# Performance work log

Measured on AMD Instinct MI355X. Metric: run time of the kernel, lower is better.

## Reference

```python
import jax, jax.numpy as jnp
import numpy as np

N, H, S, R, T = 32768, 512, 8, 64, 12

def setup_inputs() -> dict:
    key = jax.random.key(0)
    ks = jax.random.split(key, 7)
    scale = 1.0 / np.sqrt(H)
    return {
        "encodings": jax.random.normal(ks[0], (N, H), dtype=jnp.float32),
        "domain_encs": jax.random.normal(ks[1], (S, H), dtype=jnp.float32),
        "Us": jax.random.normal(ks[2], (S, H, R), dtype=jnp.float32) * scale,
        "W1": jax.random.normal(ks[3], (S, H, H), dtype=jnp.float32) * scale,
        "b1": jax.random.normal(ks[4], (S, H), dtype=jnp.float32) * 0.01,
        "W2": jax.random.normal(ks[5], (S, H, T), dtype=jnp.float32) * scale,
        "b2": jax.random.normal(ks[6], (S, T), dtype=jnp.float32) * 0.01,
    }

def reference(encodings, domain_encs, Us, W1, b1, W2, b2):
    # Mahalanobis soft routing. Original computes (p-mu) @ (U U^T) @ (p-mu)^T
    # and takes sqrt(diag) -- algebraically identical to project-then-square-sum.
    diff = encodings[None, :, :] - domain_encs[:, None, :]        # [S, N, H]
    proj = jnp.einsum('snh,shr->snr', diff, Us)                   # [S, N, R]
    dist = jnp.sqrt(jnp.sum(proj * proj, axis=-1))                # [S, N]
    alphas = jax.nn.softmax(-dist, axis=0)                        # softmax over sources

    # Per-source classifier: Dropout(eval=identity) -> ReLU -> Linear(H,H)
    # -> Dropout -> ReLU -> Linear(H,T) -> Sigmoid
    h0 = jax.nn.relu(encodings)                                   # [N, H]
    h1 = jax.nn.relu(jnp.einsum('nh,shk->snk', h0, W1) + b1[:, None, :])  # [S, N, H]
    out = jax.nn.sigmoid(jnp.einsum('snk,skt->snt', h1, W2) + b2[:, None, :])  # [S, N, T]

    # Softmax-weighted combine of expert outputs
    return jnp.sum(alphas[:, :, None] * out, axis=0)              # [N, T]
```

## Files before the change

kernel.cpp:

```cpp
#include <hip/hip_runtime.h>
#include <hip/hip_bf16.h>

typedef unsigned short u16;
typedef __bf16 bf16x8 __attribute__((ext_vector_type(8)));
typedef float f32x4 __attribute__((ext_vector_type(4)));

#define NROWS 32768
#define H 512
#define NS 8
#define NR 64
#define NT 12

#define WS_W1T   0
#define WS_UCT   4194304
#define WS_W2T   4718592
#define WS_CVEC  4849664
#define WS_ALPH  4851712

union BFU { __bf16 h; u16 u; };
__device__ __forceinline__ u16 f2bf(float v) { BFU b; b.h = (__bf16)v; return b.u; }

__device__ __forceinline__ void gload16(const u16* g, u16* l) {
  __builtin_amdgcn_global_load_lds(
      (const __attribute__((address_space(1))) unsigned int*)g,
      (__attribute__((address_space(3))) unsigned int*)l, 16, 0, 0);
}

__global__ __launch_bounds__(256) void prep(
    const float* __restrict__ W1, u16* __restrict__ W1T,
    const float* __restrict__ Us, u16* __restrict__ UcatT,
    const float* __restrict__ W2, u16* __restrict__ W2T,
    const float* __restrict__ mu, float* __restrict__ cvec) {
  __shared__ float tile[32][33];
  const int bid = blockIdx.x;
  const int tx = threadIdx.x, ty = threadIdx.y;
  if (bid < 2432) {
    const float* in; u16* out; int Rr, Cc, Cpad, b, r0, c0;
    if (bid < 2048) {
      in = W1; out = W1T; Rr = 512; Cc = 512; Cpad = 512;
      r0 = (bid & 15) * 32; c0 = ((bid >> 4) & 15) * 32; b = bid >> 8;
    } else if (bid < 2304) {
      int t2 = bid - 2048; in = Us; out = UcatT; Rr = 512; Cc = 64; Cpad = 64;
      r0 = (t2 & 15) * 32; c0 = ((t2 >> 4) & 1) * 32; b = t2 >> 5;
    } else {
      int t2 = bid - 2304; in = W2; out = W2T; Rr = 512; Cc = 12; Cpad = 16;
      r0 = (t2 & 15) * 32; c0 = 0; b = t2 >> 4;
    }
#pragma unroll
    for (int i = 0; i < 4; i++) {
      int r = r0 + ty + i * 8, c = c0 + tx;
      float v = 0.f;
      if (r < Rr && c < Cc) v = in[((size_t)b * Rr + r) * Cc + c];
      tile[ty + i * 8][tx] = v;
    }
    __syncthreads();
#pragma unroll
    for (int i = 0; i < 4; i++) {
      int c = c0 + ty + i * 8, r = r0 + tx;
      if (c < Cpad && r < Rr) out[((size_t)b * Cpad + c) * Rr + r] = f2bf(tile[tx][ty + i * 8]);
    }
  } else {
    const int tid = ty * 32 + tx;
    const int idx = (bid - 2432) * 4 + (tid >> 6);
    const int s = idx >> 6, r = idx & 63, t = tid & 63;
    float acc = 0.f;
#pragma unroll
    for (int k = t; k < H; k += 64) acc += mu[s * H + k] * Us[((size_t)s * H + k) * NR + r];
#pragma unroll
    for (int m = 32; m; m >>= 1) acc += __shfl_xor(acc, m, 64);
    if (t == 0) cvec[idx] = acc;
  }
}

__device__ __forceinline__ void stage32r(const u16* __restrict__ g, u16* l, int wave, int lane) {
#pragma unroll
  for (int i = 0; i < 8; i++) {
    int r = wave * 8 + i;
    gload16(g + (size_t)r * 512 + (size_t)((lane ^ (r & 7)) * 8), l + r * 512);
  }
}

__global__ __launch_bounds__(256, 2) void routing(
    const float* __restrict__ enc, const u16* __restrict__ UcatT,
    const float* __restrict__ cvec, float* __restrict__ alphT) {
  __shared__ __align__(16) u16 Wst[2][32 * 512];
  __shared__ float distS[NS][64];

  const int tid = threadIdx.x;
  const int wave = tid >> 6, lane = tid & 63;
  const int lnm = lane & 15, lnq = lane >> 4;
  const int row0 = blockIdx.x * 64;

  bf16x8 afrag[16];
  {
    const float* rp = enc + (size_t)(row0 + wave * 16 + lnm) * H + lnq * 8;
#pragma unroll
    for (int ks = 0; ks < 16; ks++) {
      float4 x0 = *(const float4*)(rp + ks * 32);
      float4 x1 = *(const float4*)(rp + ks * 32 + 4);
      bf16x8 a;
      a[0] = (__bf16)x0.x; a[1] = (__bf16)x0.y; a[2] = (__bf16)x0.z; a[3] = (__bf16)x0.w;
      a[4] = (__bf16)x1.x; a[5] = (__bf16)x1.y; a[6] = (__bf16)x1.z; a[7] = (__bf16)x1.w;
      afrag[ks] = a;
    }
  }

  stage32r(UcatT, Wst[0], wave, lane);
  float dsq[4] = {0.f, 0.f, 0.f, 0.f};
#pragma unroll 1
  for (int q = 0; q < 16; q++) {
    int s = q >> 1, half = q & 1;
    __syncthreads();
    if (q < 15) stage32r(UcatT + (size_t)(q + 1) * 32 * 512, Wst[(q + 1) & 1], wave, lane);
    const u16* buf = Wst[q & 1];
    f32x4 acc[2] = {};
#pragma unroll
    for (int ks = 0; ks < 16; ks++) {
      int uu = ((ks * 4 + lnq) ^ (lnm & 7)) * 8;
      bf16x8 b0 = *(const bf16x8*)&buf[lnm * 512 + uu];
      bf16x8 b1v = *(const bf16x8*)&buf[(16 + lnm) * 512 + uu];
      acc[0] = __builtin_amdgcn_mfma_f32_16x16x32_bf16(afrag[ks], b0, acc[0], 0, 0, 0);
      acc[1] = __builtin_amdgcn_mfma_f32_16x16x32_bf16(afrag[ks], b1v, acc[1], 0, 0, 0);
    }
#pragma unroll
    for (int ct = 0; ct < 2; ct++) {
      float cv = cvec[s * 64 + half * 32 + ct * 16 + lnm];
#pragma unroll
      for (int g = 0; g < 4; g++) { float d = acc[ct][g] - cv; dsq[g] += d * d; }
    }
    if (half == 1) {
#pragma unroll
      for (int m = 1; m < 16; m <<= 1) {
#pragma unroll
        for (int g = 0; g < 4; g++) dsq[g] += __shfl_xor(dsq[g], m, 16);
      }
      if (lnm == 0) {
#pragma unroll
        for (int g = 0; g < 4; g++) distS[s][wave * 16 + lnq * 4 + g] = sqrtf(dsq[g]);
      }
#pragma unroll
      for (int g = 0; g < 4; g++) dsq[g] = 0.f;
    }
  }
  __syncthreads();
  if (tid < 64) {
    float dmin = distS[0][tid];
#pragma unroll
    for (int s = 1; s < NS; s++) dmin = fminf(dmin, distS[s][tid]);
    float den = 0.f, e[NS];
#pragma unroll
    for (int s = 0; s < NS; s++) { e[s] = __expf(dmin - distS[s][tid]); den += e[s]; }
    float inv = 1.f / den;
#pragma unroll
    for (int s = 0; s < NS; s++) alphT[(size_t)s * NROWS + row0 + tid] = e[s] * inv;
  }
}

#define H1STR 40

__device__ __forceinline__ void stageW16(const u16* __restrict__ g, u16* l, int tid) {
#pragma unroll
  for (int i = 0; i < 4; i++) {
    int flat = tid + i * 256;
    int r = flat >> 5, u = flat & 31;
    gload16(g + (size_t)r * 512 + (u ^ (r & 7)) * 8, l + flat * 8);
  }
}

__device__ __forceinline__ const u16* chunk_base(const u16* W1g, int q) {
  return W1g + ((size_t)(q >> 5) * 512 + ((q >> 1) & 15) * 32) * 512 + (q & 1) * 256;
}

__global__ __launch_bounds__(256, 2) void moe_main(
    const float* __restrict__ enc, const u16* __restrict__ W1T,
    const u16* __restrict__ W2T, const float* __restrict__ alphT,
    const float* __restrict__ b1g, const float* __restrict__ b2g,
    float* __restrict__ out) {
  __shared__ __align__(16) u16 Wst[3][32 * 256];
  __shared__ __align__(16) u16 h1c[128 * H1STR];
  __shared__ float alphS[4][128];

  const int tid = threadIdx.x;
  const int wave = tid >> 6, lane = tid & 63;
  const int lnm = lane & 15, lnq = lane >> 4;
  const int rb = blockIdx.x >> 1, sg = blockIdx.x & 1;
  const int row0 = rb * 128, sbase = sg * 4;

#pragma unroll
  for (int i = 0; i < 2; i++) {
    int u = tid + i * 256, j = u >> 7, r = u & 127;
    alphS[j][r] = alphT[(size_t)(sbase + j) * NROWS + row0 + r];
  }

  float b2v[4];
#pragma unroll
  for (int j = 0; j < 4; j++) b2v[j] = (lnm < NT) ? b2g[(sbase + j) * NT + lnm] : 0.f;

  bf16x8 efrag[2][16];
#pragma unroll
  for (int t = 0; t < 2; t++) {
    const float* rp = enc + (size_t)(row0 + wave * 32 + t * 16 + lnm) * H + lnq * 8;
#pragma unroll
    for (int ks = 0; ks < 16; ks++) {
      float4 x0 = *(const float4*)(rp + ks * 32);
      float4 x1 = *(const float4*)(rp + ks * 32 + 4);
      bf16x8 a;
      a[0] = (__bf16)fmaxf(x0.x, 0.f); a[1] = (__bf16)fmaxf(x0.y, 0.f);
      a[2] = (__bf16)fmaxf(x0.z, 0.f); a[3] = (__bf16)fmaxf(x0.w, 0.f);
      a[4] = (__bf16)fmaxf(x1.x, 0.f); a[5] = (__bf16)fmaxf(x1.y, 0.f);
      a[6] = (__bf16)fmaxf(x1.z, 0.f); a[7] = (__bf16)fmaxf(x1.w, 0.f);
      efrag[t][ks] = a;
    }
  }

  __syncthreads();

  const u16* W1g = W1T + (size_t)sbase * 512 * 512;
  stageW16(chunk_base(W1g, 0), Wst[0], tid);
  int cb = 0;
  f32x4 acc[2][2];
  float fin[2][4] = {};
  const int stg = wave & 1;
#pragma unroll 1
  for (int j = 0; j < 4; j++) {
    const int s = sbase + j;
    f32x4 oacc[2] = {};
#pragma unroll 1
    for (int wc = 0; wc < 16; wc++) {
      const int q = j * 32 + wc * 2;
      float4 bq0 = *(const float4*)&b1g[s * H + wc * 32 + lnq * 4];
      float4 bq1 = *(const float4*)&b1g[s * H + wc * 32 + 16 + lnq * 4];
      bf16x8 bw = *(const bf16x8*)&W2T[((size_t)s * 16 + lnm) * H + wc * 32 + lnq * 8];
      asm volatile("" ::: "memory");
      {
        const int nb = (cb == 2) ? 0 : cb + 1;
        stageW16(chunk_base(W1g, q + 1), Wst[nb], tid);
        asm volatile("s_waitcnt vmcnt(7)" ::: "memory");
        __builtin_amdgcn_s_barrier();
        const u16* buf = Wst[cb];
#pragma unroll
        for (int t = 0; t < 2; t++) { acc[t][0] = (f32x4){0,0,0,0}; acc[t][1] = (f32x4){0,0,0,0}; }
        __builtin_amdgcn_s_setprio(1);
        if (stg == 0) {
#pragma unroll
          for (int ks = 0; ks < 8; ks++) {
            const int uu = ((ks * 4 + lnq) ^ (lnm & 7)) * 8;
            bf16x8 w0 = *(const bf16x8*)&buf[lnm * 256 + uu];
            bf16x8 w1 = *(const bf16x8*)&buf[(16 + lnm) * 256 + uu];
#pragma unroll
            for (int t = 0; t < 2; t++) {
              acc[t][0] = __builtin_amdgcn_mfma_f32_16x16x32_bf16(w0, efrag[t][ks], acc[t][0], 0, 0, 0);
              acc[t][1] = __builtin_amdgcn_mfma_f32_16x16x32_bf16(w1, efrag[t][ks], acc[t][1], 0, 0, 0);
            }
          }
        } else {
#pragma unroll
          for (int ki = 0; ki < 8; ki++) {
            const int ks = ki ^ 1;
            const int uu = ((ks * 4 + lnq) ^ (lnm & 7)) * 8;
            bf16x8 w0 = *(const bf16x8*)&buf[lnm * 256 + uu];
            bf16x8 w1 = *(const bf16x8*)&buf[(16 + lnm) * 256 + uu];
#pragma unroll
            for (int t = 0; t < 2; t++) {
              acc[t][0] = __builtin_amdgcn_mfma_f32_16x16x32_bf16(w0, efrag[t][ks], acc[t][0], 0, 0, 0);
              acc[t][1] = __builtin_amdgcn_mfma_f32_16x16x32_bf16(w1, efrag[t][ks], acc[t][1], 0, 0, 0);
            }
          }
        }
        __builtin_amdgcn_s_setprio(0);
        cb = nb;
      }
      {
        const int nb = (cb == 2) ? 0 : cb + 1;
        if (q + 2 < 128) {
          stageW16(chunk_base(W1g, q + 2), Wst[nb], tid);
          asm volatile("s_waitcnt vmcnt(4)" ::: "memory");
        } else {
          asm volatile("s_waitcnt vmcnt(0)" ::: "memory");
        }
        __builtin_amdgcn_s_barrier();
        const u16* buf = Wst[cb];
        __builtin_amdgcn_s_setprio(1);
        if (stg == 0) {
#pragma unroll
          for (int ks = 0; ks < 8; ks++) {
            const int uu = ((ks * 4 + lnq) ^ (lnm & 7)) * 8;
            bf16x8 w0 = *(const bf16x8*)&buf[lnm * 256 + uu];
            bf16x8 w1 = *(const bf16x8*)&buf[(16 + lnm) * 256 + uu];
#pragma unroll
            for (int t = 0; t < 2; t++) {
              acc[t][0] = __builtin_amdgcn_mfma_f32_16x16x32_bf16(w0, efrag[t][8 + ks], acc[t][0], 0, 0, 0);
              acc[t][1] = __builtin_amdgcn_mfma_f32_16x16x32_bf16(w1, efrag[t][8 + ks], acc[t][1], 0, 0, 0);
            }
          }
        } else {
#pragma unroll
          for (int ki = 0; ki < 8; ki++) {
            const int ks = ki ^ 1;
            const int uu = ((ks * 4 + lnq) ^ (lnm & 7)) * 8;
            bf16x8 w0 = *(const bf16x8*)&buf[lnm * 256 + uu];
            bf16x8 w1 = *(const bf16x8*)&buf[(16 + lnm) * 256 + uu];
#pragma unroll
            for (int t = 0; t < 2; t++) {
              acc[t][0] = __builtin_amdgcn_mfma_f32_16x16x32_bf16(w0, efrag[t][8 + ks], acc[t][0], 0, 0, 0);
              acc[t][1] = __builtin_amdgcn_mfma_f32_16x16x32_bf16(w1, efrag[t][8 + ks], acc[t][1], 0, 0, 0);
            }
          }
        }
        __builtin_amdgcn_s_setprio(0);
        cb = nb;
      }
#pragma unroll
      for (int ct = 0; ct < 2; ct++) {
        float4 bq = ct ? bq1 : bq0;
#pragma unroll
        for (int t = 0; t < 2; t++) {
          union { u16 u[4]; uint2 v; } pk;
          pk.u[0] = f2bf(fmaxf(acc[t][ct][0] + bq.x, 0.f));
          pk.u[1] = f2bf(fmaxf(acc[t][ct][1] + bq.y, 0.f));
          pk.u[2] = f2bf(fmaxf(acc[t][ct][2] + bq.z, 0.f));
          pk.u[3] = f2bf(fmaxf(acc[t][ct][3] + bq.w, 0.f));
          *(uint2*)&h1c[(wave * 32 + t * 16 + lnm) * H1STR + ct * 16 + lnq * 4] = pk.v;
        }
      }
      {
#pragma unroll
        for (int t = 0; t < 2; t++) {
          bf16x8 a2 = *(const bf16x8*)&h1c[(wave * 32 + t * 16 + lnm) * H1STR + lnq * 8];
          oacc[t] = __builtin_amdgcn_mfma_f32_16x16x32_bf16(a2, bw, oacc[t], 0, 0, 0);
        }
      }
    }
    {
#pragma unroll
      for (int t = 0; t < 2; t++) {
#pragma unroll
        for (int g = 0; g < 4; g++) {
          float sig = 1.f / (1.f + __expf(-(oacc[t][g] + b2v[j])));
          fin[t][g] += alphS[j][wave * 32 + t * 16 + lnq * 4 + g] * sig;
        }
      }
    }
  }
  if (lnm < NT) {
#pragma unroll
    for (int t = 0; t < 2; t++) {
#pragma unroll
      for (int g = 0; g < 4; g++) {
        int rg = row0 + wave * 32 + t * 16 + lnq * 4 + g;
        atomicAdd(&out[(size_t)rg * NT + lnm], fin[t][g]);
      }
    }
  }
}

extern "C" void kernel_launch(void* const* d_in, const int* in_sizes, int n_in,
                              void* d_out, int out_size, void* d_ws, size_t ws_size,
                              hipStream_t stream) {
  const float* enc = (const float*)d_in[0];
  const float* mu  = (const float*)d_in[1];
  const float* Us  = (const float*)d_in[2];
  const float* W1  = (const float*)d_in[3];
  const float* b1  = (const float*)d_in[4];
  const float* W2  = (const float*)d_in[5];
  const float* b2  = (const float*)d_in[6];
  float* out = (float*)d_out;
  char* ws = (char*)d_ws;
  u16* W1T    = (u16*)(ws + WS_W1T);
  u16* UcatT  = (u16*)(ws + WS_UCT);
  u16* W2T    = (u16*)(ws + WS_W2T);
  float* cvec = (float*)(ws + WS_CVEC);
  float* alphT = (float*)(ws + WS_ALPH);

  prep<<<2560, dim3(32, 8, 1), 0, stream>>>(W1, W1T, Us, UcatT, W2, W2T, mu, cvec);
  routing<<<512, 256, 0, stream>>>(enc, UcatT, cvec, alphT);
  hipMemsetAsync(out, 0, (size_t)out_size * sizeof(float), stream);
  moe_main<<<512, 256, 0, stream>>>(enc, W1T, W2T, alphT, b1, b2, out);
}
```

Before: 276.3 us.

## Triple-buffer routing weight staging with half-K chunks and cache cvec in LDS

The routing kernel now stages the U weights in half-width 32x256 chunks through a three-slot ring, using a vmcnt wait plus a raw barrier instead of a __syncthreads per double-buffered step. The cvec centre projections are also preloaded into shared memory. This is meant to overlap global-to-LDS loads with MFMA work more deeply and to remove the per-iteration global reads. Separately, moe_main drops the per-wave alternating ks order (ki^1), which had been used to spread out LDS bank access, and goes back to a single uniform loop. That may bring back LDS conflicts but removes branch duplication.

Result: no change. 273.1 us (-1.1%).

```diff
diff --git a/kernel.cpp b/kernel.cpp
--- a/kernel.cpp
+++ b/kernel.cpp
@@ -72,24 +72,29 @@
   }
 }
 
-__device__ __forceinline__ void stage32r(const u16* __restrict__ g, u16* l, int wave, int lane) {
-#pragma unroll
-  for (int i = 0; i < 8; i++) {
-    int r = wave * 8 + i;
-    gload16(g + (size_t)r * 512 + (size_t)((lane ^ (r & 7)) * 8), l + r * 512);
+__device__ __forceinline__ void stageW16(const u16* __restrict__ g, u16* l, int tid) {
+#pragma unroll
+  for (int i = 0; i < 4; i++) {
+    int flat = tid + i * 256;
+    int r = flat >> 5, u = flat & 31;
+    gload16(g + (size_t)r * 512 + (u ^ (r & 7)) * 8, l + flat * 8);
   }
 }
 
 __global__ __launch_bounds__(256, 2) void routing(
     const float* __restrict__ enc, const u16* __restrict__ UcatT,
     const float* __restrict__ cvec, float* __restrict__ alphT) {
-  __shared__ __align__(16) u16 Wst[2][32 * 512];
+  __shared__ __align__(16) u16 Wst[3][32 * 256];
   __shared__ float distS[NS][64];
+  __shared__ float cvS[512];
 
   const int tid = threadIdx.x;
   const int wave = tid >> 6, lane = tid & 63;
   const int lnm = lane & 15, lnq = lane >> 4;
   const int row0 = blockIdx.x * 64;
+
+  cvS[tid] = cvec[tid];
+  cvS[256 + tid] = cvec[256 + tid];
 
   bf16x8 afrag[16];
   {
@@ -105,30 +110,45 @@
     }
   }
 
-  stage32r(UcatT, Wst[0], wave, lane);
+  __syncthreads();
+
+  stageW16(UcatT, Wst[0], tid);
+  int cb = 0;
   float dsq[4] = {0.f, 0.f, 0.f, 0.f};
 #pragma unroll 1
-  for (int q = 0; q < 16; q++) {
-    int s = q >> 1, half = q & 1;
-    __syncthreads();
-    if (q < 15) stage32r(UcatT + (size_t)(q + 1) * 32 * 512, Wst[(q + 1) & 1], wave, lane);
-    const u16* buf = Wst[q & 1];
+  for (int wcw = 0; wcw < 16; wcw++) {
     f32x4 acc[2] = {};
 #pragma unroll
-    for (int ks = 0; ks < 16; ks++) {
-      int uu = ((ks * 4 + lnq) ^ (lnm & 7)) * 8;
-      bf16x8 b0 = *(const bf16x8*)&buf[lnm * 512 + uu];
-      bf16x8 b1v = *(const bf16x8*)&buf[(16 + lnm) * 512 + uu];
-      acc[0] = __builtin_amdgcn_mfma_f32_16x16x32_bf16(afrag[ks], b0, acc[0], 0, 0, 0);
-      acc[1] = __builtin_amdgcn_mfma_f32_16x16x32_bf16(afrag[ks], b1v, acc[1], 0, 0, 0);
+    for (int kh = 0; kh < 2; kh++) {
+      const int q = wcw * 2 + kh;
+      const int nb = (cb == 2) ? 0 : cb + 1;
+      if (q + 1 < 32) {
+        stageW16(UcatT + (size_t)((q + 1) >> 1) * 32 * 512 + ((q + 1) & 1) * 256, Wst[nb], tid);
+        asm volatile("s_waitcnt vmcnt(4)" ::: "memory");
+      } else {
+        asm volatile("s_waitcnt vmcnt(0)" ::: "memory");
+      }
+      __builtin_amdgcn_s_barrier();
+      const u16* buf = Wst[cb];
+      __builtin_amdgcn_s_setprio(1);
+#pragma unroll
+      for (int ks = 0; ks < 8; ks++) {
+        const int uu = ((ks * 4 + lnq) ^ (lnm & 7)) * 8;
+        bf16x8 b0 = *(const bf16x8*)&buf[lnm * 256 + uu];
+        bf16x8 b1v = *(const bf16x8*)&buf[(16 + lnm) * 256 + uu];
+        acc[0] = __builtin_amdgcn_mfma_f32_16x16x32_bf16(afrag[kh * 8 + ks], b0, acc[0], 0, 0, 0);
+        acc[1] = __builtin_amdgcn_mfma_f32_16x16x32_bf16(afrag[kh * 8 + ks], b1v, acc[1], 0, 0, 0);
+      }
+      __builtin_amdgcn_s_setprio(0);
+      cb = nb;
     }
 #pragma unroll
     for (int ct = 0; ct < 2; ct++) {
-      float cv = cvec[s * 64 + half * 32 + ct * 16 + lnm];
+      float cv = cvS[wcw * 32 + ct * 16 + lnm];
 #pragma unroll
       for (int g = 0; g < 4; g++) { float d = acc[ct][g] - cv; dsq[g] += d * d; }
     }
-    if (half == 1) {
+    if (wcw & 1) {
 #pragma unroll
       for (int m = 1; m < 16; m <<= 1) {
 #pragma unroll
@@ -136,7 +156,7 @@
       }
       if (lnm == 0) {
 #pragma unroll
-        for (int g = 0; g < 4; g++) distS[s][wave * 16 + lnq * 4 + g] = sqrtf(dsq[g]);
+        for (int g = 0; g < 4; g++) distS[wcw >> 1][wave * 16 + lnq * 4 + g] = sqrtf(dsq[g]);
       }
 #pragma unroll
       for (int g = 0; g < 4; g++) dsq[g] = 0.f;
@@ -157,15 +177,6 @@
 }
 
 #define H1STR 40
-
-__device__ __forceinline__ void stageW16(const u16* __restrict__ g, u16* l, int tid) {
-#pragma unroll
-  for (int i = 0; i < 4; i++) {
-    int flat = tid + i * 256;
-    int r = flat >> 5, u = flat & 31;
-    gload16(g + (size_t)r * 512 + (u ^ (r & 7)) * 8, l + flat * 8);
-  }
-}
 
 __device__ __forceinline__ const u16* chunk_base(const u16* W1g, int q) {
   return W1g + ((size_t)(q >> 5) * 512 + ((q >> 1) & 15) * 32) * 512 + (q & 1) * 256;
@@ -220,7 +231,6 @@
   int cb = 0;
   f32x4 acc[2][2];
   float fin[2][4] = {};
-  const int stg = wave & 1;
 #pragma unroll 1
   for (int j = 0; j < 4; j++) {
     const int s = sbase + j;
@@ -241,30 +251,15 @@
 #pragma unroll
         for (int t = 0; t < 2; t++) { acc[t][0] = (f32x4){0,0,0,0}; acc[t][1] = (f32x4){0,0,0,0}; }
         __builtin_amdgcn_s_setprio(1);
-        if (stg == 0) {
-#pragma unroll
-          for (int ks = 0; ks < 8; ks++) {
-            const int uu = ((ks * 4 + lnq) ^ (lnm & 7)) * 8;
-            bf16x8 w0 = *(const bf16x8*)&buf[lnm * 256 + uu];
-            bf16x8 w1 = *(const bf16x8*)&buf[(16 + lnm) * 256 + uu];
-#pragma unroll
-            for (int t = 0; t < 2; t++) {
-              acc[t][0] = __builtin_amdgcn_mfma_f32_16x16x32_bf16(w0, efrag[t][ks], acc[t][0], 0, 0, 0);
-              acc[t][1] = __builtin_amdgcn_mfma_f32_16x16x32_bf16(w1, efrag[t][ks], acc[t][1], 0, 0, 0);
-            }
-          }
-        } else {
-#pragma unroll
-          for (int ki = 0; ki < 8; ki++) {
-            const int ks = ki ^ 1;
-            const int uu = ((ks * 4 + lnq) ^ (lnm & 7)) * 8;
-            bf16x8 w0 = *(const bf16x8*)&buf[lnm * 256 + uu];
-            bf16x8 w1 = *(const bf16x8*)&buf[(16 + lnm) * 256 + uu];
-#pragma unroll
-            for (int t = 0; t < 2; t++) {
-              acc[t][0] = __builtin_amdgcn_mfma_f32_16x16x32_bf16(w0, efrag[t][ks], acc[t][0], 0, 0, 0);
-              acc[t][1] = __builtin_amdgcn_mfma_f32_16x16x32_bf16(w1, efrag[t][ks], acc[t][1], 0, 0, 0);
-            }
+#pragma unroll
+        for (int ks = 0; ks < 8; ks++) {
+          const int uu = ((ks * 4 + lnq) ^ (lnm & 7)) * 8;
+          bf16x8 w0 = *(const bf16x8*)&buf[lnm * 256 + uu];
+          bf16x8 w1 = *(const bf16x8*)&buf[(16 + lnm) * 256 + uu];
+#pragma unroll
+          for (int t = 0; t < 2; t++) {
+            acc[t][0] = __builtin_amdgcn_mfma_f32_16x16x32_bf16(w0, efrag[t][ks], acc[t][0], 0, 0, 0);
+            acc[t][1] = __builtin_amdgcn_mfma_f32_16x16x32_bf16(w1, efrag[t][ks], acc[t][1], 0, 0, 0);
           }
         }
         __builtin_amdgcn_s_setprio(0);
@@ -281,30 +276,15 @@
         __builtin_amdgcn_s_barrier();
         const u16* buf = Wst[cb];
         __builtin_amdgcn_s_setprio(1);
-        if (stg == 0) {
-#pragma unroll
-          for (int ks = 0; ks < 8; ks++) {
-            const int uu = ((ks * 4 + lnq) ^ (lnm & 7)) * 8;
-            bf16x8 w0 = *(const bf16x8*)&buf[lnm * 256 + uu];
-            bf16x8 w1 = *(const bf16x8*)&buf[(16 + lnm) * 256 + uu];
-#pragma unroll
-            for (int t = 0; t < 2; t++) {
-              acc[t][0] = __builtin_amdgcn_mfma_f32_16x16x32_bf16(w0, efrag[t][8 + ks], acc[t][0], 0, 0, 0);
-              acc[t][1] = __builtin_amdgcn_mfma_f32_16x16x32_bf16(w1, efrag[t][8 + ks], acc[t][1], 0, 0, 0);
-            }
-          }
-        } else {
-#pragma unroll
-          for (int ki = 0; ki < 8; ki++) {
-            const int ks = ki ^ 1;
-            const int uu = ((ks * 4 + lnq) ^ (lnm & 7)) * 8;
-            bf16x8 w0 = *(const bf16x8*)&buf[lnm * 256 + uu];
-            bf16x8 w1 = *(const bf16x8*)&buf[(16 + lnm) * 256 + uu];
-#pragma unroll
-            for (int t = 0; t < 2; t++) {
-              acc[t][0] = __builtin_amdgcn_mfma_f32_16x16x32_bf16(w0, efrag[t][8 + ks], acc[t][0], 0, 0, 0);
-              acc[t][1] = __builtin_amdgcn_mfma_f32_16x16x32_bf16(w1, efrag[t][8 + ks], acc[t][1], 0, 0, 0);
-            }
+#pragma unroll
+        for (int ks = 0; ks < 8; ks++) {
+          const int uu = ((ks * 4 + lnq) ^ (lnm & 7)) * 8;
+          bf16x8 w0 = *(const bf16x8*)&buf[lnm * 256 + uu];
+          bf16x8 w1 = *(const bf16x8*)&buf[(16 + lnm) * 256 + uu];
+#pragma unroll
+          for (int t = 0; t < 2; t++) {
+            acc[t][0] = __builtin_amdgcn_mfma_f32_16x16x32_bf16(w0, efrag[t][8 + ks], acc[t][0], 0, 0, 0);
+            acc[t][1] = __builtin_amdgcn_mfma_f32_16x16x32_bf16(w1, efrag[t][8 + ks], acc[t][1], 0, 0, 0);
           }
         }
         __builtin_amdgcn_s_setprio(0);
```
